# Kernel optimization log

Measured on AMD Instinct MI355X. Metric: run time of the kernel, lower is better.

The kernel has to match this reference:

```python
import jax, jax.numpy as jnp
import numpy as np

B, S, D, H = 8, 1024, 256, 8


def setup_inputs() -> dict:
    key = jax.random.key(0)
    ks = jax.random.split(key, 8)
    scale = 0.02
    return {
        "x": jax.random.normal(ks[0], (B, S, D), dtype=jnp.float32),
        "Wq": jax.random.normal(ks[1], (H, D, D), dtype=jnp.float32) * scale,
        "Wk": jax.random.normal(ks[2], (H, D, D), dtype=jnp.float32) * scale,
        "Wv": jax.random.normal(ks[3], (H, D, D), dtype=jnp.float32) * scale,
        "bq": jax.random.normal(ks[4], (H, D), dtype=jnp.float32) * scale,
        "bk": jax.random.normal(ks[5], (H, D), dtype=jnp.float32) * scale,
        "bv": jax.random.normal(ks[6], (H, D), dtype=jnp.float32) * scale,
        "Wp": jax.random.normal(ks[7], (D, H * D), dtype=jnp.float32) * scale,
    }


def reference(x, Wq, Wk, Wv, bq, bk, bv, Wp):
    # Per-head Linear layers, vectorized over the head axis.
    # torch Linear: y = x @ W.T + b, W shape [out, in] -> einsum 'bsd,hed->bhse'
    q = jnp.einsum('bsd,hed->bhse', x, Wq) + bq[:, None, :]   # [B,H,S,D]
    k = jnp.einsum('bsd,hed->bhse', x, Wk) + bk[:, None, :]
    v = jnp.einsum('bsd,hed->bhse', x, Wv) + bv[:, None, :]
    d = x.shape[-1]
    scores = jnp.einsum('bhse,bhte->bhst', q, k) / jnp.sqrt(jnp.float32(d))
    attn = jax.nn.softmax(scores, axis=-1)                    # softmax over keys (dim=2 per head)
    o = jnp.einsum('bhst,bhte->bhse', attn, v)                # [B,H,S,D]
    # concat heads along feature dim (head order preserved)
    o = o.transpose(0, 2, 1, 3).reshape(x.shape[0], x.shape[1], -1)  # [B,S,H*D]
    return o @ Wp.T                                           # bias-free projection [B,S,D]
```

## Files before the change

### kernel.cpp

```cpp
#include <hip/hip_runtime.h>

typedef unsigned short u16;
typedef __attribute__((ext_vector_type(4)))  float f32x4;
typedef __attribute__((ext_vector_type(16))) float f32x16;
typedef __attribute__((ext_vector_type(8)))  short s16x8;
typedef __attribute__((ext_vector_type(4)))  unsigned short u16x4;

typedef const __attribute__((address_space(1))) void* gp1;
typedef __attribute__((address_space(3))) void* lp3;
#define GLOAD16(g, l) __builtin_amdgcn_global_load_lds((gp1)(g), (lp3)(l), 16, 0, 0)

__device__ __forceinline__ u16 f2bf(float f) {
    union { float f; unsigned u; } c; c.f = f;
    unsigned r = c.u + 0x7fffu + ((c.u >> 16) & 1u);
    return (u16)(r >> 16);
}

__global__ void castall(const float* __restrict__ x,  const float* __restrict__ wq,
                        const float* __restrict__ wk, const float* __restrict__ wv,
                        const float* __restrict__ wp,
                        u16* __restrict__ xb,  u16* __restrict__ wqb, u16* __restrict__ wkb,
                        u16* __restrict__ wvb, u16* __restrict__ wpb) {
    int blk = blockIdx.x;
    const float* src; u16* dst; long off;
    if (blk < 2048) { src = x; dst = xb; off = (long)blk * 1024; }
    else {
        int w = (blk - 2048) >> 9, bb = (blk - 2048) & 511;
        src = (w == 0 ? wq : w == 1 ? wk : w == 2 ? wv : wp);
        dst = (w == 0 ? wqb : w == 1 ? wkb : w == 2 ? wvb : wpb);
        off = (long)bb * 1024;
    }
    long i = off + threadIdx.x * 4;
    f32x4 v = *(const f32x4*)(src + i);
    u16x4 o;
    o[0] = f2bf(v[0]); o[1] = f2bf(v[1]); o[2] = f2bf(v[2]); o[3] = f2bf(v[3]);
    *(u16x4*)(dst + i) = o;
}

__global__ __launch_bounds__(256) void qkv_gemm(
    const u16* __restrict__ xb,
    const u16* __restrict__ Wqb, const u16* __restrict__ Wkb, const u16* __restrict__ Wvb,
    const float* __restrict__ bq, const float* __restrict__ bk, const float* __restrict__ bv,
    u16* __restrict__ Qb, u16* __restrict__ Kimg, u16* __restrict__ Vimg)
{
    __shared__ u16 As[128 * 32];
    __shared__ u16 Bs[128 * 32];
    const int tid  = threadIdx.x;
    const int lane = tid & 63;
    const int li   = lane & 15, lg = lane >> 4;
    const int wave = tid >> 6;
    const int wr   = wave >> 1, wc = wave & 1;
    const int m0   = blockIdx.x * 128;
    const int n0g  = blockIdx.y * 128;
    const int w    = n0g >> 11;
    const int h    = (n0g >> 8) & 7;
    const int e0   = n0g & 255;
    const u16* Wsel = (w == 0 ? Wqb : (w == 1 ? Wkb : Wvb)) + h * 65536;

    const int srow = tid >> 2;
    const int scol = (tid & 3) * 8;

    f32x4 acc[4][4] = {};

    for (int k0 = 0; k0 < 256; k0 += 32) {
        __syncthreads();
        #pragma unroll
        for (int i = 0; i < 2; ++i) {
            int row = i * 64 + srow;
            GLOAD16(&xb[(m0 + row) * 256 + k0 + scol],   &As[i * 2048 + tid * 8]);
            GLOAD16(&Wsel[(e0 + row) * 256 + k0 + scol], &Bs[i * 2048 + tid * 8]);
        }
        __syncthreads();
        s16x8 af[4], bf[4];
        #pragma unroll
        for (int mi = 0; mi < 4; ++mi)
            af[mi] = *(const s16x8*)&As[(wr * 64 + mi * 16 + li) * 32 + lg * 8];
        #pragma unroll
        for (int ni = 0; ni < 4; ++ni)
            bf[ni] = *(const s16x8*)&Bs[(wc * 64 + ni * 16 + li) * 32 + lg * 8];
        #pragma unroll
        for (int mi = 0; mi < 4; ++mi)
            #pragma unroll
            for (int ni = 0; ni < 4; ++ni)
                acc[mi][ni] = __builtin_amdgcn_mfma_f32_16x16x32_bf16(af[mi], bf[ni], acc[mi][ni], 0, 0, 0);
    }

    const int b  = m0 >> 10;
    const int s0 = m0 & 1023;
    if (w == 0) {
        const float* bp = bq + 256 * h;
        #pragma unroll
        for (int ni = 0; ni < 4; ++ni) {
            const int e = e0 + wc * 64 + ni * 16 + li;
            const float bias = bp[e];
            u16* obase = Qb + ((size_t)(b * 8 + h)) * 1024 * 256 + e;
            #pragma unroll
            for (int mi = 0; mi < 4; ++mi)
                #pragma unroll
                for (int r = 0; r < 4; ++r) {
                    int s = s0 + wr * 64 + mi * 16 + lg * 4 + r;
                    obase[(size_t)s * 256] = f2bf(acc[mi][ni][r] + bias);
                }
        }
    } else if (w == 1) {
        const float* bp = bk + 256 * h;
        u16* kb = Kimg + ((size_t)(b * 8 + h)) * 262144;
        #pragma unroll
        for (int ni = 0; ni < 4; ++ni) {
            const int e = e0 + wc * 64 + ni * 16 + li;
            const float bias = bp[e];
            #pragma unroll
            for (int mi = 0; mi < 4; ++mi)
                #pragma unroll
                for (int r = 0; r < 4; ++r) {
                    int s = s0 + wr * 64 + mi * 16 + lg * 4 + r;
                    int t = s >> 5, rr = s & 31;
                    size_t idx = (size_t)t * 8192 + rr * 256
                               + (((e & ~7) ^ ((rr & 7) << 3)) | (e & 7));
                    kb[idx] = f2bf(acc[mi][ni][r] + bias);
                }
        }
    } else {
        const float* bp = bv + 256 * h;
        u16* vb = Vimg + ((size_t)(b * 8 + h)) * 327680;
        #pragma unroll
        for (int ni = 0; ni < 4; ++ni) {
            const int e = e0 + wc * 64 + ni * 16 + li;
            const float bias = bp[e];
            #pragma unroll
            for (int mi = 0; mi < 4; ++mi) {
                int s = s0 + wr * 64 + mi * 16 + lg * 4;
                int t = s >> 5, cj = s & 31;
                size_t idx = (size_t)t * 10240 + e * 40 + cj;
                u16x4 pk;
                #pragma unroll
                for (int r = 0; r < 4; ++r) pk[r] = f2bf(acc[mi][ni][r] + bias);
                *(u16x4*)&vb[idx] = pk;
            }
        }
    }
}

__device__ __forceinline__ void softmax_pack(
    f32x16& sacc, float& m_run, float& l_run, f32x16* oacc,
    int hi, s16x8& paA, s16x8& paB)
{
    const float C = 0.09016844f;
    const float THR = 16.0f;
    float pm;
    {
        float t[8];
        #pragma unroll
        for (int r = 0; r < 8; ++r) t[r] = fmaxf(sacc[r], sacc[r + 8]);
        #pragma unroll
        for (int r = 0; r < 4; ++r) t[r] = fmaxf(t[r], t[r + 4]);
        t[0] = fmaxf(t[0], t[2]); t[1] = fmaxf(t[1], t[3]);
        pm = fmaxf(t[0], t[1]);
    }
    pm = fmaxf(pm, __shfl_xor(pm, 32));
    if (!__all(pm - m_run <= THR)) {
        const float mnew = fmaxf(m_run, pm);
        const float corr = __builtin_amdgcn_exp2f((m_run - mnew) * C);
        l_run *= corr;
        #pragma unroll
        for (int r = 0; r < 16; ++r) {
            float rc = __shfl(corr, (r & 3) + 8 * (r >> 2) + 4 * hi);
            #pragma unroll
            for (int et = 0; et < 8; ++et) oacc[et][r] *= rc;
        }
        m_run = mnew;
    }
    #pragma unroll
    for (int r = 0; r < 16; ++r)
        sacc[r] = __builtin_amdgcn_exp2f((sacc[r] - m_run) * C);
    float psum;
    {
        float s[8];
        #pragma unroll
        for (int r = 0; r < 8; ++r) s[r] = sacc[r] + sacc[r + 8];
        #pragma unroll
        for (int r = 0; r < 4; ++r) s[r] = s[r] + s[r + 4];
        psum = (s[0] + s[1]) + (s[2] + s[3]);
    }
    psum += __shfl_xor(psum, 32);
    l_run += psum;
    unsigned dwA[4], dwB[4];
    #pragma unroll
    for (int c = 0; c < 4; ++c) {
        asm("v_cvt_pk_bf16_f32 %0, %1, %2" : "=v"(dwA[c]) : "v"(sacc[4*c]),   "v"(sacc[4*c+1]));
        asm("v_cvt_pk_bf16_f32 %0, %1, %2" : "=v"(dwB[c]) : "v"(sacc[4*c+2]), "v"(sacc[4*c+3]));
    }
    {
        unsigned a0 = dwA[0], a1 = dwA[1], b0 = dwB[0], b1 = dwB[1];
        asm("v_permlane32_swap_b32 %0, %1" : "+v"(a0), "+v"(a1));
        asm("v_permlane32_swap_b32 %0, %1" : "+v"(b0), "+v"(b1));
        union { unsigned u[4]; s16x8 v; } pk;
        pk.u[0] = a0; pk.u[1] = b0; pk.u[2] = a1; pk.u[3] = b1;
        paA = pk.v;
    }
    {
        unsigned a0 = dwA[2], a1 = dwA[3], b0 = dwB[2], b1 = dwB[3];
        asm("v_permlane32_swap_b32 %0, %1" : "+v"(a0), "+v"(a1));
        asm("v_permlane32_swap_b32 %0, %1" : "+v"(b0), "+v"(b1));
        union { unsigned u[4]; s16x8 v; } pk;
        pk.u[0] = a0; pk.u[1] = b0; pk.u[2] = a1; pk.u[3] = b1;
        paB = pk.v;
    }
}

__device__ __forceinline__ void attn_body(
    const int i, const u16* __restrict__ kt, const u16* __restrict__ vt,
    const s16x8 (&qf)[16], const int col, const int hi, const int ksw,
    f32x16* oacc, float& m_run, float& l_run, s16x8& paA, s16x8& paB)
{
    const int hi8 = hi * 8;
    f32x16 sacc = (f32x16){};
    __builtin_amdgcn_s_setprio(1);
    {
        const int rb_ = col * 256;
        #pragma unroll
        for (int dk = 0; dk < 16; ++dk) {
            s16x8 kf = *(const s16x8*)&kt[rb_ + ((dk * 16 + hi8) ^ ksw)];
            sacc = __builtin_amdgcn_mfma_f32_32x32x16_bf16(kf, qf[dk], sacc, 0, 0, 0);
        }
    }
    if (i > 0) {
        #pragma unroll
        for (int et = 0; et < 8; ++et) {
            s16x8 vf = *(const s16x8*)&vt[(et * 32 + col) * 40 + hi8];
            oacc[et] = __builtin_amdgcn_mfma_f32_32x32x16_bf16(paA, vf, oacc[et], 0, 0, 0);
        }
        #pragma unroll
        for (int et = 0; et < 8; ++et) {
            s16x8 vf = *(const s16x8*)&vt[(et * 32 + col) * 40 + 16 + hi8];
            oacc[et] = __builtin_amdgcn_mfma_f32_32x32x16_bf16(paB, vf, oacc[et], 0, 0, 0);
        }
    }
    __builtin_amdgcn_s_setprio(0);
    softmax_pack(sacc, m_run, l_run, oacc, hi, paA, paB);
}

__global__ __launch_bounds__(512, 2) void attn(
    const u16* __restrict__ Qb, const u16* __restrict__ Kimg,
    const u16* __restrict__ Vimg, u16* __restrict__ Ob)
{
    __shared__ u16 kbuf[3][8192];
    __shared__ u16 vbuf[3][10240];
    const int tid  = threadIdx.x;
    const int lane = tid & 63;
    const int wave = tid >> 6;
    const int col  = lane & 31;
    const int hi   = lane >> 5;
    const int hi8  = hi * 8;
    const int ksw  = (lane & 7) << 3;
    const int bid  = ((blockIdx.x & 7) << 5) | (blockIdx.x >> 3);
    const int bh   = bid >> 2;
    const int qblk = bid & 3;
    const int q0   = qblk * 256 + wave * 32;

    const u16* qp = Qb + ((size_t)bh * 1024 + q0) * 256;
    const u16* kg = Kimg + (size_t)bh * 262144;
    const u16* vg = Vimg + (size_t)bh * 327680;

    #define STAGEK(sl, t)                                                         \
        {                                                                         \
            const int s_ = (sl), t_ = (t);                                        \
            const size_t kb_ = (size_t)t_ * 8192 + tid * 8;                       \
            _Pragma("unroll")                                                     \
            for (int c_ = 0; c_ < 4; ++c_)                                        \
                GLOAD16(&kg[kb_ + c_ * 2048], &kbuf[s_][c_ * 2048 + tid * 8]);    \
        }
    #define STAGEV(sl, t)                                                         \
        {                                                                         \
            const int s_ = (sl), t_ = (t);                                        \
            const int vth_ = tid - 256;                                          \
            const size_t vb_ = (size_t)t_ * 10240 + vth_ * 8;                     \
            _Pragma("unroll")                                                     \
            for (int c_ = 0; c_ < 5; ++c_)                                        \
                GLOAD16(&vg[vb_ + c_ * 2048], &vbuf[s_][c_ * 2048 + vth_ * 8]);   \
        }

    s16x8 qf[16];
    #pragma unroll
    for (int dk = 0; dk < 16; ++dk)
        qf[dk] = *(const s16x8*)&qp[(size_t)col * 256 + dk * 16 + hi8];

    if (tid < 256) { STAGEK(0, 0); STAGEK(1, 1); STAGEK(2, 2); }
    else           { STAGEV(0, 0); STAGEV(1, 1); }

    f32x16 oacc[8] = {};
    float m_run = -1e30f, l_run = 0.f;
    s16x8 paA = {}, paB = {};

    for (int i = 0; i < 32; ++i) {
        if (tid < 256) { asm volatile("s_waitcnt vmcnt(8)"  ::: "memory"); }
        else           { asm volatile("s_waitcnt vmcnt(10)" ::: "memory"); }
        __builtin_amdgcn_s_barrier();
        asm volatile("" ::: "memory");
        const int ks = i % 3;
        const int vs = (i + 2) % 3;
        attn_body(i, kbuf[ks], vbuf[vs], qf, col, hi, ksw,
                  oacc, m_run, l_run, paA, paB);
        asm volatile("" ::: "memory");
        __builtin_amdgcn_s_barrier();
        asm volatile("" ::: "memory");
        const int ktile = (i + 3 < 32) ? (i + 3) : 31;
        const int vtile = (i + 2 < 32) ? (i + 2) : 31;
        if (tid < 256) { STAGEK(ks, ktile); }
        else           { STAGEV(vs, vtile); }
    }
    #undef STAGEK
    #undef STAGEV

    if (tid >= 256) { asm volatile("s_waitcnt vmcnt(10)" ::: "memory"); }
    __builtin_amdgcn_s_barrier();
    asm volatile("" ::: "memory");
    {
        const u16* vt = vbuf[1];
        __builtin_amdgcn_s_setprio(1);
        #pragma unroll
        for (int et = 0; et < 8; ++et) {
            s16x8 vf = *(const s16x8*)&vt[(et * 32 + col) * 40 + hi8];
            oacc[et] = __builtin_amdgcn_mfma_f32_32x32x16_bf16(paA, vf, oacc[et], 0, 0, 0);
        }
        #pragma unroll
        for (int et = 0; et < 8; ++et) {
            s16x8 vf = *(const s16x8*)&vt[(et * 32 + col) * 40 + 16 + hi8];
            oacc[et] = __builtin_amdgcn_mfma_f32_32x32x16_bf16(paB, vf, oacc[et], 0, 0, 0);
        }
        __builtin_amdgcn_s_setprio(0);
    }

    const float linv = 1.0f / l_run;
    const int b = bh >> 3, h = bh & 7;
    u16* op = Ob + ((size_t)b * 1024) * 2048 + h * 256;
    #pragma unroll
    for (int r = 0; r < 16; ++r) {
        const int crow = (r & 3) + 8 * (r >> 2) + 4 * hi;
        float lr = __shfl(linv, crow);
        const size_t row = q0 + crow;
        #pragma unroll
        for (int et = 0; et < 8; ++et)
            op[row * 2048 + et * 32 + col] = f2bf(oacc[et][r] * lr);
    }
}

__global__ __launch_bounds__(256) void out_gemm(
    const u16* __restrict__ Ob, const u16* __restrict__ Wpb, float* __restrict__ out)
{
    __shared__ u16 As[32 * 32];
    __shared__ u16 Bs[128 * 32];
    const int tid  = threadIdx.x;
    const int lane = tid & 63;
    const int li   = lane & 15, lg = lane >> 4;
    const int wave = tid >> 6;
    const int wr   = wave >> 1, wc = wave & 1;
    const int m0   = blockIdx.x * 32;
    const int n0   = blockIdx.y * 128;
    const int srow = tid >> 2;
    const int scol = (tid & 3) * 8;

    f32x4 acc[4] = {};

    for (int k0 = 0; k0 < 2048; k0 += 32) {
        __syncthreads();
        if (tid < 128)
            GLOAD16(&Ob[(size_t)(m0 + srow) * 2048 + k0 + scol], &As[tid * 8]);
        #pragma unroll
        for (int i = 0; i < 2; ++i)
            GLOAD16(&Wpb[(size_t)(n0 + i * 64 + srow) * 2048 + k0 + scol],
                    &Bs[i * 2048 + tid * 8]);
        __syncthreads();
        s16x8 af, bf[4];
        af = *(const s16x8*)&As[(wr * 16 + li) * 32 + lg * 8];
        #pragma unroll
        for (int ni = 0; ni < 4; ++ni)
            bf[ni] = *(const s16x8*)&Bs[(wc * 64 + ni * 16 + li) * 32 + lg * 8];
        #pragma unroll
        for (int ni = 0; ni < 4; ++ni)
            acc[ni] = __builtin_amdgcn_mfma_f32_16x16x32_bf16(af, bf[ni], acc[ni], 0, 0, 0);
    }

    #pragma unroll
    for (int ni = 0; ni < 4; ++ni) {
        int n = n0 + wc * 64 + ni * 16 + li;
        #pragma unroll
        for (int r = 0; r < 4; ++r) {
            int m = m0 + wr * 16 + lg * 4 + r;
            out[(size_t)m * 256 + n] = acc[ni][r];
        }
    }
}

extern "C" void kernel_launch(void* const* d_in, const int* in_sizes, int n_in,
                              void* d_out, int out_size, void* d_ws, size_t ws_size,
                              hipStream_t stream) {
    const float* x  = (const float*)d_in[0];
    const float* Wq = (const float*)d_in[1];
    const float* Wk = (const float*)d_in[2];
    const float* Wv = (const float*)d_in[3];
    const float* bq = (const float*)d_in[4];
    const float* bk = (const float*)d_in[5];
    const float* bv = (const float*)d_in[6];
    const float* Wp = (const float*)d_in[7];
    float* out = (float*)d_out;

    u16* xb   = (u16*)d_ws;
    u16* Wqb  = xb   + (1u << 21);
    u16* Wkb  = Wqb  + (1u << 19);
    u16* Wvb  = Wkb  + (1u << 19);
    u16* Wpb  = Wvb  + (1u << 19);
    u16* Qb   = Wpb  + (1u << 19);
    u16* Kimg = Qb   + (1u << 24);
    u16* Vimg = Kimg + (1u << 24);
    u16* Ob   = Vimg + 20971520u;

    castall<<<4096, 256, 0, stream>>>(x, Wq, Wk, Wv, Wp, xb, Wqb, Wkb, Wvb, Wpb);
    qkv_gemm<<<dim3(64, 48), 256, 0, stream>>>(xb, Wqb, Wkb, Wvb, bq, bk, bv, Qb, Kimg, Vimg);
    attn<<<256, 512, 0, stream>>>(Qb, Kimg, Vimg, Ob);
    out_gemm<<<dim3(256, 2), 256, 0, stream>>>(Ob, Wpb, out);
}
```

Baseline: 167.2 us.

## Software-pipeline softmax one tile behind QK and drop the second barrier

Restructures the attention loop so the softmax of the previous score tile runs before the current QK^T MFMAs, letting softmax VALU work overlap matrix work. It also removes the trailing barrier per iteration by issuing the next K/V prefetch right after the single barrier. Prefetch depth shrinks by one tile (K two ahead, V one ahead) with adjusted vmcnt waits. The shallower prefetch may expose more memory latency, and holding an extra score accumulator raises register pressure.

After: 226.8 us. 1.36x slower.

```diff
diff --git a/kernel.cpp b/kernel.cpp
--- a/kernel.cpp
+++ b/kernel.cpp
@@ -208,38 +208,6 @@
     }
 }
 
-__device__ __forceinline__ void attn_body(
-    const int i, const u16* __restrict__ kt, const u16* __restrict__ vt,
-    const s16x8 (&qf)[16], const int col, const int hi, const int ksw,
-    f32x16* oacc, float& m_run, float& l_run, s16x8& paA, s16x8& paB)
-{
-    const int hi8 = hi * 8;
-    f32x16 sacc = (f32x16){};
-    __builtin_amdgcn_s_setprio(1);
-    {
-        const int rb_ = col * 256;
-        #pragma unroll
-        for (int dk = 0; dk < 16; ++dk) {
-            s16x8 kf = *(const s16x8*)&kt[rb_ + ((dk * 16 + hi8) ^ ksw)];
-            sacc = __builtin_amdgcn_mfma_f32_32x32x16_bf16(kf, qf[dk], sacc, 0, 0, 0);
-        }
-    }
-    if (i > 0) {
-        #pragma unroll
-        for (int et = 0; et < 8; ++et) {
-            s16x8 vf = *(const s16x8*)&vt[(et * 32 + col) * 40 + hi8];
-            oacc[et] = __builtin_amdgcn_mfma_f32_32x32x16_bf16(paA, vf, oacc[et], 0, 0, 0);
-        }
-        #pragma unroll
-        for (int et = 0; et < 8; ++et) {
-            s16x8 vf = *(const s16x8*)&vt[(et * 32 + col) * 40 + 16 + hi8];
-            oacc[et] = __builtin_amdgcn_mfma_f32_32x32x16_bf16(paB, vf, oacc[et], 0, 0, 0);
-        }
-    }
-    __builtin_amdgcn_s_setprio(0);
-    softmax_pack(sacc, m_run, l_run, oacc, hi, paA, paB);
-}
-
 __global__ __launch_bounds__(512, 2) void attn(
     const u16* __restrict__ Qb, const u16* __restrict__ Kimg,
     const u16* __restrict__ Vimg, u16* __restrict__ Ob)
@@ -273,7 +241,7 @@
     #define STAGEV(sl, t)                                                         \
         {                                                                         \
             const int s_ = (sl), t_ = (t);                                        \
-            const int vth_ = tid - 256;                                          \
+            const int vth_ = tid - 256;                                           \
             const size_t vb_ = (size_t)t_ * 10240 + vth_ * 8;                     \
             _Pragma("unroll")                                                     \
             for (int c_ = 0; c_ < 5; ++c_)                                        \
@@ -284,37 +252,67 @@
     #pragma unroll
     for (int dk = 0; dk < 16; ++dk)
         qf[dk] = *(const s16x8*)&qp[(size_t)col * 256 + dk * 16 + hi8];
-
-    if (tid < 256) { STAGEK(0, 0); STAGEK(1, 1); STAGEK(2, 2); }
-    else           { STAGEV(0, 0); STAGEV(1, 1); }
+    asm volatile("s_waitcnt vmcnt(0)" ::: "memory");
+
+    if (tid < 256) { STAGEK(0, 0); STAGEK(1, 1); }
+    else           { STAGEV(0, 0); }
 
     f32x16 oacc[8] = {};
     float m_run = -1e30f, l_run = 0.f;
-    s16x8 paA = {}, paB = {};
+    f32x16 sprev;
+    s16x8 paA, paB;
 
     for (int i = 0; i < 32; ++i) {
-        if (tid < 256) { asm volatile("s_waitcnt vmcnt(8)"  ::: "memory"); }
-        else           { asm volatile("s_waitcnt vmcnt(10)" ::: "memory"); }
+        if (tid < 256) { asm volatile("s_waitcnt vmcnt(4)" ::: "memory"); }
+        else           { asm volatile("s_waitcnt vmcnt(5)" ::: "memory"); }
         __builtin_amdgcn_s_barrier();
         asm volatile("" ::: "memory");
-        const int ks = i % 3;
-        const int vs = (i + 2) % 3;
-        attn_body(i, kbuf[ks], vbuf[vs], qf, col, hi, ksw,
-                  oacc, m_run, l_run, paA, paB);
+
+        const int ktile = (i + 2 < 32) ? (i + 2) : 31;
+        const int vtile = (i + 1 < 32) ? (i + 1) : 31;
+        if (tid < 256) { STAGEK((i + 2) % 3, ktile); }
+        else           { STAGEV((i + 1) % 3, vtile); }
+
+        const u16* kt = kbuf[i % 3];
+        const u16* vt = vbuf[(i + 2) % 3];
+
+        if (i > 0)
+            softmax_pack(sprev, m_run, l_run, oacc, hi, paA, paB);
+
+        f32x16 scur = (f32x16){};
+        __builtin_amdgcn_s_setprio(1);
+        {
+            const int rb_ = col * 256;
+            #pragma unroll
+            for (int dk = 0; dk < 16; ++dk) {
+                s16x8 kf = *(const s16x8*)&kt[rb_ + ((dk * 16 + hi8) ^ ksw)];
+                scur = __builtin_amdgcn_mfma_f32_32x32x16_bf16(kf, qf[dk], scur, 0, 0, 0);
+            }
+        }
+        if (i > 0) {
+            #pragma unroll
+            for (int et = 0; et < 8; ++et) {
+                s16x8 vf = *(const s16x8*)&vt[(et * 32 + col) * 40 + hi8];
+                oacc[et] = __builtin_amdgcn_mfma_f32_32x32x16_bf16(paA, vf, oacc[et], 0, 0, 0);
+            }
+            #pragma unroll
+            for (int et = 0; et < 8; ++et) {
+                s16x8 vf = *(const s16x8*)&vt[(et * 32 + col) * 40 + 16 + hi8];
+                oacc[et] = __builtin_amdgcn_mfma_f32_32x32x16_bf16(paB, vf, oacc[et], 0, 0, 0);
+            }
+        }
+        __builtin_amdgcn_s_setprio(0);
+
+        sprev = scur;
         asm volatile("" ::: "memory");
-        __builtin_amdgcn_s_barrier();
-        asm volatile("" ::: "memory");
-        const int ktile = (i + 3 < 32) ? (i + 3) : 31;
-        const int vtile = (i + 2 < 32) ? (i + 2) : 31;
-        if (tid < 256) { STAGEK(ks, ktile); }
-        else           { STAGEV(vs, vtile); }
     }
     #undef STAGEK
     #undef STAGEV
 
-    if (tid >= 256) { asm volatile("s_waitcnt vmcnt(10)" ::: "memory"); }
+    if (tid >= 256) { asm volatile("s_waitcnt vmcnt(5)" ::: "memory"); }
     __builtin_amdgcn_s_barrier();
     asm volatile("" ::: "memory");
+    softmax_pack(sprev, m_run, l_run, oacc, hi, paA, paB);
     {
         const u16* vt = vbuf[1];
         __builtin_amdgcn_s_setprio(1);
```
